# Kernel tuning notes

Measured on AMD Instinct MI355X. Metric: run time of the kernel, lower is better.

## Reference

```python
import jax, jax.numpy as jnp
import numpy as np

RANK = 24          # init: rank
WHITEN = True      # init: whiten
NS_ITERS = 5       # Newton-Schulz iterations for inverse matrix square root
EPS = 1e-5         # covariance jitter


def _ns_inv_sqrt(C, iters=NS_ITERS):
    # Newton-Schulz iteration computing C^{-1/2} for SPD C: (B, N, N).
    N = C.shape[-1]
    I = jnp.eye(N, dtype=C.dtype)
    normC = jnp.sqrt(jnp.sum(C * C, axis=(-2, -1), keepdims=True))  # Frobenius norm
    Y = C / normC
    Z = jnp.broadcast_to(I, C.shape)
    for _ in range(iters):
        T = 0.5 * (3.0 * I - Z @ Y)
        Y = Y @ T
        Z = T @ Z
    return Z / jnp.sqrt(normC)  # Z -> norm^{1/2} * C^{-1/2}


def _whiten(X):
    # X: (B, n, N) -> X @ Cov(X)^{-1/2}
    n = X.shape[-2]
    N = X.shape[-1]
    C = jnp.einsum('bnd,bne->bde', X, X) / n + EPS * jnp.eye(N, dtype=X.dtype)
    return X @ _ns_inv_sqrt(C)


def _procrustes_rotation(M):
    # M = S^T T (B, d, d); orthogonal R = U Vh minimizing ||S R - T||_F (Kabsch).
    U, _, Vh = jnp.linalg.svd(M, full_matrices=False)
    return U @ Vh


def _align(source, target, rank=RANK, whiten=WHITEN):
    S = _whiten(source) if whiten else source
    T = _whiten(target) if whiten else target
    N = S.shape[-1]
    if N <= 32:
        # full Procrustes
        R = _procrustes_rotation(jnp.einsum('bnd,bne->bde', S, T))
        aligned = S @ R
    else:
        # project to rank-r joint subspace, align there, lift back with
        # identity on the orthogonal complement: R = Q Rr Q^T + (I - Q Q^T)
        X = jnp.concatenate([S, T], axis=1)                 # (B, 2n, N)
        _, _, Vh = jnp.linalg.svd(X, full_matrices=False)    # Vh: (B, N', N)
        Q = jnp.swapaxes(Vh[:, :rank, :], -2, -1)            # (B, N, r)
        Sp = S @ Q                                           # (B, n, r)
        Tp = T @ Q
        Rr = _procrustes_rotation(jnp.einsum('bnr,bns->brs', Sp, Tp))  # (B, r, r) small SVD
        # aligned = S @ (Q Rr Q^T + I - Q Q^T) = S + Sp (Rr - I) Q^T
        aligned = S + Sp @ (Rr - jnp.eye(rank, dtype=S.dtype)) @ jnp.swapaxes(Q, -2, -1)
    return aligned


def setup_inputs() -> dict:
    key = jax.random.key(0)
    k1, k2 = jax.random.split(key)
    source = jax.random.normal(k1, (64, 512, 384), dtype=jnp.float32)
    target = jax.random.normal(k2, (64, 512, 384), dtype=jnp.float32)
    return {"source": source, "target": target}


def reference(source, target):
    aligned = _align(source, target)
    # diagnostic: mean cosine similarity between aligned and target rows
    cos = jnp.sum(aligned * target, axis=-1) / (
        jnp.linalg.norm(aligned, axis=-1) * jnp.linalg.norm(target, axis=-1) + 1e-8)
    cos_after = jnp.mean(cos)
    return aligned, cos_after
```

## Files before the change

### kernel.cpp

```cpp
#include <hip/hip_runtime.h>
#include <math.h>

static constexpr int BATCH = 64;
static constexpr int NR  = 512;
static constexpr int ND  = 384;
static constexpr int RK  = 24;
static constexpr int POLAR_ITERS = 36;
static constexpr int PNB = 32;
static constexpr long SZC = (long)BATCH * ND * ND;
static constexpr int SSTR = BATCH * RK;

#define MODE_PLAIN 0
#define MODE_COV   1
#define MODE_SCALE 3
#define MODE_ACC   4

typedef _Float16 half8 __attribute__((ext_vector_type(8)));
typedef _Float16 half4 __attribute__((ext_vector_type(4)));
typedef float floatx4 __attribute__((ext_vector_type(4)));

template<int TA>
__global__ __launch_bounds__(256)
void gemm_kernel(const float* __restrict__ Ag, const float* __restrict__ Bg,
                 float* __restrict__ Cg, int M, int N, int K,
                 long sA, long sB, long sC, int lda, int ldb, int ldc,
                 int mode, const float* __restrict__ scale, int sym, int tmask)
{
    const int batch = blockIdx.y;
    const int tilesN = N >> 7;
    int ti, tj;
    if (sym) {
        int idx = blockIdx.x;
        ti = 0; int rem = tilesN;
        while (idx >= rem) { idx -= rem; ti++; rem--; }
        tj = ti + idx;
    } else {
        tj = blockIdx.x % tilesN;
        ti = blockIdx.x / tilesN;
    }
    const int n0 = tj * 128, m0 = ti * 128;
    const float* A = Ag + (long)batch * sA;
    const float* Bm = Bg + (long)batch * sB;
    float* C = Cg + (long)batch * sC;

    __shared__ _Float16 Ah[128][40], Al[128][40];
    __shared__ _Float16 Bh[128][40], Bl[128][40];

    const int tid = threadIdx.x;
    const int wave = tid >> 6, lane = tid & 63;
    const int wm0 = (wave >> 1) * 64, wn0 = (wave & 1) * 64;
    const int fm = lane & 15;
    const int fq = lane >> 4;

    floatx4 acc[4][4];
#pragma unroll
    for (int i = 0; i < 4; i++)
#pragma unroll
        for (int j = 0; j < 4; j++) acc[i][j] = (floatx4){0.f, 0.f, 0.f, 0.f};

    for (int k0 = 0; k0 < K; k0 += 32) {
        if (TA == 0) {
#pragma unroll
            for (int q = 0; q < 4; q++) {
                int idx = tid + q * 256;
                int row = idx >> 3, kq = (idx & 7) * 4;
                float4 v = *(const float4*)&A[(long)(m0 + row) * lda + k0 + kq];
                if (tmask & 1) {
                    int gr = m0 + row, gc = k0 + kq;
                    v.x = ((gr == gc    ) ? 1.5f : 0.f) - 0.5f * v.x;
                    v.y = ((gr == gc + 1) ? 1.5f : 0.f) - 0.5f * v.y;
                    v.z = ((gr == gc + 2) ? 1.5f : 0.f) - 0.5f * v.z;
                    v.w = ((gr == gc + 3) ? 1.5f : 0.f) - 0.5f * v.w;
                }
                _Float16 h0 = (_Float16)v.x; _Float16 l0 = (_Float16)(v.x - (float)h0);
                _Float16 h1 = (_Float16)v.y; _Float16 l1 = (_Float16)(v.y - (float)h1);
                _Float16 h2 = (_Float16)v.z; _Float16 l2 = (_Float16)(v.z - (float)h2);
                _Float16 h3 = (_Float16)v.w; _Float16 l3 = (_Float16)(v.w - (float)h3);
                half4 hv, lv;
                hv[0] = h0; hv[1] = h1; hv[2] = h2; hv[3] = h3;
                lv[0] = l0; lv[1] = l1; lv[2] = l2; lv[3] = l3;
                *(half4*)&Ah[row][kq] = hv;
                *(half4*)&Al[row][kq] = lv;
            }
        } else {
            int m = tid & 127, kb = (tid >> 7) * 16;
            _Float16 hbuf[16], lbuf[16];
#pragma unroll
            for (int i = 0; i < 16; i++) {
                float v = A[(long)(k0 + kb + i) * lda + m0 + m];
                _Float16 hh = (_Float16)v;
                hbuf[i] = hh; lbuf[i] = (_Float16)(v - (float)hh);
            }
#pragma unroll
            for (int i = 0; i < 16; i += 4) {
                half4 hv, lv;
                hv[0] = hbuf[i]; hv[1] = hbuf[i + 1]; hv[2] = hbuf[i + 2]; hv[3] = hbuf[i + 3];
                lv[0] = lbuf[i]; lv[1] = lbuf[i + 1]; lv[2] = lbuf[i + 2]; lv[3] = lbuf[i + 3];
                *(half4*)&Ah[m][kb + i] = hv;
                *(half4*)&Al[m][kb + i] = lv;
            }
        }
        {
            int n = tid & 127, kb = (tid >> 7) * 16;
            _Float16 hbuf[16], lbuf[16];
#pragma unroll
            for (int i = 0; i < 16; i++) {
                float v = Bm[(long)(k0 + kb + i) * ldb + n0 + n];
                if (tmask & 2) v = (((k0 + kb + i) == (n0 + n)) ? 1.5f : 0.f) - 0.5f * v;
                _Float16 hh = (_Float16)v;
                hbuf[i] = hh; lbuf[i] = (_Float16)(v - (float)hh);
            }
#pragma unroll
            for (int i = 0; i < 16; i += 4) {
                half4 hv, lv;
                hv[0] = hbuf[i]; hv[1] = hbuf[i + 1]; hv[2] = hbuf[i + 2]; hv[3] = hbuf[i + 3];
                lv[0] = lbuf[i]; lv[1] = lbuf[i + 1]; lv[2] = lbuf[i + 2]; lv[3] = lbuf[i + 3];
                *(half4*)&Bh[n][kb + i] = hv;
                *(half4*)&Bl[n][kb + i] = lv;
            }
        }
        __syncthreads();

        half8 ah[4], alv[4], bh[4], blv[4];
#pragma unroll
        for (int mt = 0; mt < 4; mt++) {
            ah[mt]  = *(const half8*)&Ah[wm0 + mt * 16 + fm][fq * 8];
            alv[mt] = *(const half8*)&Al[wm0 + mt * 16 + fm][fq * 8];
        }
#pragma unroll
        for (int nt = 0; nt < 4; nt++) {
            bh[nt]  = *(const half8*)&Bh[wn0 + nt * 16 + fm][fq * 8];
            blv[nt] = *(const half8*)&Bl[wn0 + nt * 16 + fm][fq * 8];
        }
#pragma unroll
        for (int mt = 0; mt < 4; mt++) {
#pragma unroll
            for (int nt = 0; nt < 4; nt++) {
                floatx4 a = acc[mt][nt];
                a = __builtin_amdgcn_mfma_f32_16x16x32_f16(alv[mt], bh[nt], a, 0, 0, 0);
                a = __builtin_amdgcn_mfma_f32_16x16x32_f16(ah[mt], blv[nt], a, 0, 0, 0);
                a = __builtin_amdgcn_mfma_f32_16x16x32_f16(ah[mt], bh[nt], a, 0, 0, 0);
                acc[mt][nt] = a;
            }
        }
        __syncthreads();
    }

    float scl = 1.f;
    if (mode == MODE_SCALE) scl = 1.0f / sqrtf(scale[batch]);

#pragma unroll
    for (int mt = 0; mt < 4; mt++) {
#pragma unroll
        for (int nt = 0; nt < 4; nt++) {
            int gn = n0 + wn0 + nt * 16 + fm;
#pragma unroll
            for (int r = 0; r < 4; r++) {
                int gm = m0 + wm0 + mt * 16 + fq * 4 + r;
                float a = acc[mt][nt][r];
                float* cp = C + (long)gm * ldc + gn;
                float v = a;
                if (mode == MODE_COV)      v = a * (1.0f / 512.0f) + ((gm == gn) ? 1e-5f : 0.f);
                else if (mode == MODE_SCALE) v = a * scl;
                else if (mode == MODE_ACC) v = a + *cp;
                *cp = v;
                if (sym && ti != tj) {
                    float* cq = C + (long)gn * ldc + gm;
                    float vq = v;
                    if (mode == MODE_ACC) vq = a + *cq;
                    *cq = vq;
                }
            }
        }
    }
}

__global__ __launch_bounds__(256)
void frob_kernel(const float* __restrict__ Cm, float* __restrict__ nrm)
{
    int b = blockIdx.x;
    const float* p = Cm + (long)b * ND * ND;
    float s = 0.f;
    for (int i = threadIdx.x; i < ND * ND; i += 256) { float v = p[i]; s += v * v; }
    __shared__ float red[256];
    red[threadIdx.x] = s; __syncthreads();
    for (int off = 128; off > 0; off >>= 1) {
        if (threadIdx.x < off) red[threadIdx.x] += red[threadIdx.x + off];
        __syncthreads();
    }
    if (threadIdx.x == 0) nrm[b] = sqrtf(red[0]);
}

__global__ __launch_bounds__(256)
void initns_kernel(float* __restrict__ Mb, float* __restrict__ Z, const float* __restrict__ nrm)
{
    const int total = BATCH * ND * ND;
    for (int idx = blockIdx.x * 256 + threadIdx.x; idx < total; idx += gridDim.x * 256) {
        int b = idx / (ND * ND);
        int rem = idx - b * (ND * ND);
        int r = rem / ND, c = rem - r * ND;
        float v = Mb[idx] / nrm[b];
        Mb[idx] = v;
        Z[idx] = ((r == c) ? 1.5f : 0.f) - 0.5f * v;
    }
}

__device__ __forceinline__ float bred768(float v, float* red12, int t)
{
#pragma unroll
    for (int off = 32; off > 0; off >>= 1) v += __shfl_down(v, off);
    if ((t & 63) == 0) red12[t >> 6] = v;
    __syncthreads();
    float r = 0.f;
#pragma unroll
    for (int i = 0; i < 12; i++) r += red12[i];
    __syncthreads();
    return r;
}

__global__ __launch_bounds__(768)
void tridiag_panel(float* __restrict__ Gall, float* __restrict__ dA,
                   float* __restrict__ eA, float* __restrict__ tauA,
                   float* __restrict__ Wgall, int k0)
{
    int b = blockIdx.x;
    float* A = Gall + (long)b * ND * ND;
    float* Wg = Wgall + (long)b * (PNB * ND);
    float* d = dA + b * ND; float* e = eA + b * ND; float* tau = tauA + b * ND;
    const int t = threadIdx.x;
    const int h = (t >= ND) ? 1 : 0;
    const int c = t - h * ND;
    const int g = t % 96;
    const int s = t / 96;
    __shared__ float Ul[PNB][ND];
    __shared__ float Wl[PNB][ND];
    __shared__ float u_s[ND];
    __shared__ float pp4s[8][392];
    __shared__ float al[PNB], be[PNB];
    __shared__ float red12[12];
    __shared__ float s_tau;

    const int jcnt = min(PNB, ND - 2 - k0);

    for (int j = 0; j < jcnt; j++) {
        const int k = k0 + j;
        const int m = ND - 1 - k;
        float x = 0.f;
        if (!h && c < m) {
            const int kc = (k + 1) + c;
            x = A[(long)k * ND + kc];
#pragma unroll 4
            for (int l = 0; l < j; l++) {
                x -= Ul[l][k] * Wl[l][kc] + Wl[l][k] * Ul[l][kc];
            }
            u_s[c] = x;
        }
        float sigma = bred768(x * x, red12, t);
        if (t == 0) {
            float v0 = u_s[0];
            float normx = sqrtf(sigma);
            float alpha = (v0 >= 0.f) ? -normx : normx;
            float denom = sigma - alpha * v0;
            float tk = (denom > 1e-30f) ? 1.f / denom : 0.f;
            s_tau = tk;
            float diag = A[(long)k * ND + k];
            for (int l = 0; l < j; l++) diag -= 2.f * Ul[l][k] * Wl[l][k];
            e[k] = alpha; tau[k] = tk; d[k] = diag;
            u_s[0] = v0 - alpha;
        }
        __syncthreads();
        const float tk = s_tau;

        const int kk4 = (k + 1) & ~3;
        const int off = (k + 1) - kk4;
        const int ncol4 = 96 - (kk4 >> 2);
        if (g < ncol4) {
            const int ri0 = (m * s) >> 3;
            const int ri1 = (m * (s + 1)) >> 3;
            const float* base = A + (long)(k + 1) * ND + kk4 + 4 * g;
            floatx4 p4 = (floatx4){0.f, 0.f, 0.f, 0.f};
            int i = ri0;
            for (; i + 8 <= ri1; i += 8) {
                floatx4 a0 = *(const floatx4*)&base[(long)(i    ) * ND];
                floatx4 a1 = *(const floatx4*)&base[(long)(i + 1) * ND];
                floatx4 a2 = *(const floatx4*)&base[(long)(i + 2) * ND];
                floatx4 a3 = *(const floatx4*)&base[(long)(i + 3) * ND];
                floatx4 a4 = *(const floatx4*)&base[(long)(i + 4) * ND];
                floatx4 a5 = *(const floatx4*)&base[(long)(i + 5) * ND];
                floatx4 a6 = *(const floatx4*)&base[(long)(i + 6) * ND];
                floatx4 a7 = *(const floatx4*)&base[(long)(i + 7) * ND];
                p4 += a0 * u_s[i]     + a1 * u_s[i + 1] + a2 * u_s[i + 2] + a3 * u_s[i + 3]
                    + a4 * u_s[i + 4] + a5 * u_s[i + 5] + a6 * u_s[i + 6] + a7 * u_s[i + 7];
            }
            for (; i < ri1; i++) {
                floatx4 a0 = *(const floatx4*)&base[(long)i * ND];
                p4 += a0 * u_s[i];
            }
            *(floatx4*)&pp4s[s][4 * g] = p4;
        }
        {
            int wv = t >> 6, ln = t & 63;
            for (int l = wv; l < j; l += 12) {
                float sa = 0.f, sb = 0.f;
                const float* wrow = &Wl[l][k + 1];
                const float* urow = &Ul[l][k + 1];
                for (int i = ln; i < m; i += 64) { sa += wrow[i] * u_s[i]; sb += urow[i] * u_s[i]; }
#pragma unroll
                for (int off2 = 32; off2 > 0; off2 >>= 1) {
                    sa += __shfl_down(sa, off2); sb += __shfl_down(sb, off2);
                }
                if (ln == 0) { al[l] = sa; be[l] = sb; }
            }
        }
        __syncthreads();
        float contrib = 0.f, pc = 0.f;
        if (!h && c < m) {
            int ca = c + off;
            pc = pp4s[0][ca] + pp4s[1][ca] + pp4s[2][ca] + pp4s[3][ca]
               + pp4s[4][ca] + pp4s[5][ca] + pp4s[6][ca] + pp4s[7][ca];
            const int kc = (k + 1) + c;
#pragma unroll 4
            for (int l = 0; l < j; l++) {
                pc -= al[l] * Ul[l][kc] + be[l] * Wl[l][kc];
            }
            pc *= tk;
            contrib = u_s[c] * pc;
        }
        float dotup = bred768(contrib, red12, t);
        float sc = 0.5f * tk * dotup;
        if (!h && c < m) {
            const int kc = (k + 1) + c;
            float uv = u_s[c];
            float w = pc - sc * uv;
            Wl[j][kc] = w;
            Ul[j][kc] = uv;
            Wg[j * ND + kc] = w;
            A[(long)k * ND + kc] = uv;
        }
        __syncthreads();
    }
    if (k0 + PNB >= ND - 2 && t == 0) {
        float d0 = A[(long)(ND - 2) * ND + (ND - 2)];
        float e0 = A[(long)(ND - 2) * ND + (ND - 1)];
        float d1 = A[(long)(ND - 1) * ND + (ND - 1)];
        for (int l = 0; l < jcnt; l++) {
            float u0 = A[(long)(k0 + l) * ND + (ND - 2)];
            float u1 = A[(long)(k0 + l) * ND + (ND - 1)];
            float w0 = Wg[l * ND + (ND - 2)];
            float w1 = Wg[l * ND + (ND - 1)];
            d0 -= 2.f * u0 * w0;
            e0 -= u0 * w1 + w0 * u1;
            d1 -= 2.f * u1 * w1;
        }
        d[ND - 2] = d0; d[ND - 1] = d1; e[ND - 2] = e0;
        e[ND - 1] = 0.f; tau[ND - 2] = 0.f; tau[ND - 1] = 0.f;
    }
}

__global__ __launch_bounds__(256)
void syr2k_update(float* __restrict__ Gall, const float* __restrict__ Wgall, int k0)
{
    const int k1 = k0 + PNB;
    const int tiles = (ND - k1) >> 5;
    int b = blockIdx.y;
    int ti = blockIdx.x / tiles, tj = blockIdx.x % tiles;
    int i0 = k1 + ti * 32, c0 = k1 + tj * 32;
    float* A = Gall + (long)b * ND * ND;
    const float* Wg = Wgall + (long)b * (PNB * ND);

    __shared__ float Us[PNB][36], Ws[PNB][36], Uc[PNB][36], Wc[PNB][36];
    int t = threadIdx.x;
    for (int q = t; q < PNB * 8; q += 256) {
        int l = q >> 3, c4 = (q & 7) * 4;
        *(float4*)&Us[l][c4] = *(const float4*)&A[(long)(k0 + l) * ND + i0 + c4];
        *(float4*)&Ws[l][c4] = *(const float4*)&Wg[l * ND + i0 + c4];
        *(float4*)&Uc[l][c4] = *(const float4*)&A[(long)(k0 + l) * ND + c0 + c4];
        *(float4*)&Wc[l][c4] = *(const float4*)&Wg[l * ND + c0 + c4];
    }
    __syncthreads();
    int tr = t >> 4, tc = t & 15;
    float acc00 = 0.f, acc01 = 0.f, acc10 = 0.f, acc11 = 0.f;
#pragma unroll 4
    for (int l = 0; l < PNB; l++) {
        float ua0 = Us[l][tr * 2], ua1 = Us[l][tr * 2 + 1];
        float wa0 = Ws[l][tr * 2], wa1 = Ws[l][tr * 2 + 1];
        float ub0 = Uc[l][tc * 2], ub1 = Uc[l][tc * 2 + 1];
        float wb0 = Wc[l][tc * 2], wb1 = Wc[l][tc * 2 + 1];
        acc00 += ua0 * wb0 + wa0 * ub0;
        acc01 += ua0 * wb1 + wa0 * ub1;
        acc10 += ua1 * wb0 + wa1 * ub0;
        acc11 += ua1 * wb1 + wa1 * ub1;
    }
    {
        float* r0 = &A[(long)(i0 + tr * 2) * ND + c0 + tc * 2];
        float* r1 = r0 + ND;
        float2 o0 = *(const float2*)r0, o1 = *(const float2*)r1;
        o0.x -= acc00; o0.y -= acc01;
        o1.x -= acc10; o1.y -= acc11;
        *(float2*)r0 = o0; *(float2*)r1 = o1;
    }
}

__global__ __launch_bounds__(64)
void eigvals_kernel(const float* __restrict__ dA, const float* __restrict__ eA,
                    float* __restrict__ lamA)
{
    int b = blockIdx.x, t = threadIdx.x;
    __shared__ float2 de[ND];
    __shared__ float d_s[ND], ea[ND], red[64];
    for (int i = t; i < ND; i += 64) {
        float dv = dA[b * ND + i];
        float ev = eA[b * ND + i];
        float ep = (i > 0) ? eA[b * ND + i - 1] : 0.f;
        d_s[i] = dv; ea[i] = fabsf(ev);
        de[i] = make_float2(dv, ep * ep + 1e-38f);
    }
    __syncthreads();
    float lo = 1e30f, hi = -1e30f;
    for (int i = t; i < ND; i += 64) {
        float r = ea[i] + ((i > 0) ? ea[i - 1] : 0.f);
        lo = fminf(lo, d_s[i] - r); hi = fmaxf(hi, d_s[i] + r);
    }
    red[t] = lo; __syncthreads();
    for (int off = 32; off > 0; off >>= 1) {
        if (t < off) red[t] = fminf(red[t], red[t + off]);
        __syncthreads();
    }
    lo = red[0]; __syncthreads();
    red[t] = hi; __syncthreads();
    for (int off = 32; off > 0; off >>= 1) {
        if (t < off) red[t] = fmaxf(red[t], red[t + off]);
        __syncthreads();
    }
    hi = red[0];
    if (t < RK) {
        int idx = ND - 1 - t;
        float a = lo, c = hi;
        for (int it = 0; it < 42; it++) {
            float mid = 0.5f * (a + c);
            int cnt = 0;
            float qinv = 0.f;
            for (int i = 0; i < ND; i += 8) {
                float2 v0 = de[i    ], v1 = de[i + 1], v2 = de[i + 2], v3 = de[i + 3];
                float2 v4 = de[i + 4], v5 = de[i + 5], v6 = de[i + 6], v7 = de[i + 7];
                float q;
                q = (v0.x - mid) - v0.y * qinv; cnt += (q < 0.f); qinv = __builtin_amdgcn_rcpf(q);
                q = (v1.x - mid) - v1.y * qinv; cnt += (q < 0.f); qinv = __builtin_amdgcn_rcpf(q);
                q = (v2.x - mid) - v2.y * qinv; cnt += (q < 0.f); qinv = __builtin_amdgcn_rcpf(q);
                q = (v3.x - mid) - v3.y * qinv; cnt += (q < 0.f); qinv = __builtin_amdgcn_rcpf(q);
                q = (v4.x - mid) - v4.y * qinv; cnt += (q < 0.f); qinv = __builtin_amdgcn_rcpf(q);
                q = (v5.x - mid) - v5.y * qinv; cnt += (q < 0.f); qinv = __builtin_amdgcn_rcpf(q);
                q = (v6.x - mid) - v6.y * qinv; cnt += (q < 0.f); qinv = __builtin_amdgcn_rcpf(q);
                q = (v7.x - mid) - v7.y * qinv; cnt += (q < 0.f); qinv = __builtin_amdgcn_rcpf(q);
            }
            if (cnt > idx) c = mid; else a = mid;
        }
        lamA[b * RK + t] = 0.5f * (a + c);
    }
}

__global__ __launch_bounds__(64)
void invit_kernel(const float* __restrict__ dA, const float* __restrict__ eA,
                  const float* __restrict__ lamA, float* __restrict__ scr)
{
    int b = blockIdx.x, t = threadIdx.x;
    __shared__ float d[ND], e[ND];
    __shared__ float ua[ND][RK], ub[ND][RK], uc[ND][RK];
    __shared__ float y[ND][RK];
    for (int i = t; i < ND; i += 64) { d[i] = dA[b * ND + i]; e[i] = eA[b * ND + i]; }
    __syncthreads();
    if (t >= RK) return;
    const int s = b * RK + t;
// ... 182 lines not shown
    int b = blockIdx.x, t = threadIdx.x;
    __shared__ float Sb[128][RK + 1], Tb[128][RK + 1];
    __shared__ float Xm[RK][RK + 1], Bm[RK][RK + 1], Mm[RK][RK + 1];
    __shared__ float red[256];

    float accM[3] = {0.f, 0.f, 0.f};
    for (int c = 0; c < 4; c++) {
        for (int l = t; l < 128 * RK; l += 256) {
            int row = l / RK, colj = l - row * RK;
            Sb[row][colj] = Sp[(long)b * NR * RK + (long)(c * 128 + row) * RK + colj];
            Tb[row][colj] = Tp[(long)b * NR * RK + (long)(c * 128 + row) * RK + colj];
        }
        __syncthreads();
        for (int q = 0; q < 3; q++) {
            int e = t + q * 256;
            if (e < RK * RK) {
                int r = e / RK, s2 = e - r * RK;
                float a = 0.f;
                for (int n = 0; n < 128; n++) a += Sb[n][r] * Tb[n][s2];
                accM[q] += a;
            }
        }
        __syncthreads();
    }
    float ss = 0.f;
    for (int q = 0; q < 3; q++) {
        int e = t + q * 256;
        if (e < RK * RK) {
            int r = e / RK, s2 = e - r * RK;
            Mm[r][s2] = accM[q];
            ss += accM[q] * accM[q];
        }
    }
    red[t] = ss; __syncthreads();
    for (int off = 128; off > 0; off >>= 1) {
        if (t < off) red[t] += red[t + off];
        __syncthreads();
    }
    float fro = sqrtf(red[0]);
    float inv = (fro > 1e-30f) ? 1.f / fro : 0.f;
    for (int q = 0; q < 3; q++) {
        int e = t + q * 256;
        if (e < RK * RK) { int r = e / RK, s2 = e - r * RK; Xm[r][s2] = Mm[r][s2] * inv; }
    }
    __syncthreads();
    for (int it = 0; it < POLAR_ITERS; it++) {
        for (int q = 0; q < 3; q++) {
            int e = t + q * 256;
            if (e < RK * RK) {
                int r = e / RK, s2 = e - r * RK;
                float a = 0.f;
                for (int k = 0; k < RK; k++) a += Xm[k][r] * Xm[k][s2];
                Bm[r][s2] = a;
            }
        }
        __syncthreads();
        for (int q = 0; q < 3; q++) {
            int e = t + q * 256;
            if (e < RK * RK) {
                int r = e / RK, s2 = e - r * RK;
                float a = 0.f;
                for (int k = 0; k < RK; k++) a += Xm[r][k] * Bm[k][s2];
                Mm[r][s2] = 1.5f * Xm[r][s2] - 0.5f * a;
            }
        }
        __syncthreads();
        for (int q = 0; q < 3; q++) {
            int e = t + q * 256;
            if (e < RK * RK) { int r = e / RK, s2 = e - r * RK; Xm[r][s2] = Mm[r][s2]; }
        }
        __syncthreads();
    }
    for (int q = 0; q < 3; q++) {
        int e = t + q * 256;
        if (e < RK * RK) {
            int r = e / RK, s2 = e - r * RK;
            RmI[(long)b * RK * RK + e] = Xm[r][s2] - ((r == s2) ? 1.f : 0.f);
        }
    }
}

__global__ __launch_bounds__(256)
void align_kernel(const float* __restrict__ Sw, const float* __restrict__ Sp,
                  const float* __restrict__ RmI, const float* __restrict__ Qall,
                  float* __restrict__ out)
{
    int b = blockIdx.y;
    int r0 = blockIdx.x * 64;
    int t = threadIdx.x;
    __shared__ float Qs[ND][RK + 1];
    __shared__ float Rm[RK][RK + 1];
    __shared__ float Ss[64][RK + 1];
    __shared__ float W[64][RK + 1];

    for (int l = t; l < ND * RK; l += 256) {
        int i = l / RK, j = l - i * RK;
        Qs[i][j] = Qall[(long)b * ND * RK + l];
    }
    for (int l = t; l < RK * RK; l += 256) {
        int i = l / RK, j = l - i * RK;
        Rm[i][j] = RmI[(long)b * RK * RK + l];
    }
    for (int l = t; l < 64 * RK; l += 256) {
        int i = l / RK, j = l - i * RK;
        Ss[i][j] = Sp[(long)b * NR * RK + (long)(r0 + i) * RK + j];
    }
    __syncthreads();
    for (int l = t; l < 64 * RK; l += 256) {
        int r = l / RK, j = l - r * RK;
        float a = 0.f;
        for (int k = 0; k < RK; k++) a += Ss[r][k] * Rm[k][j];
        W[r][j] = a;
    }
    __syncthreads();
    for (int r = 0; r < 64; r++) {
        for (int c = t; c < ND; c += 256) {
            float a = Sw[(long)b * NR * ND + (long)(r0 + r) * ND + c];
            float s2 = 0.f;
#pragma unroll
            for (int j = 0; j < RK; j++) s2 += W[r][j] * Qs[c][j];
            out[(long)b * NR * ND + (long)(r0 + r) * ND + c] = a + s2;
        }
    }
}

__global__ __launch_bounds__(256)
void cos_kernel(const float* __restrict__ out, const float* __restrict__ tgt,
                float* __restrict__ acc)
{
    int row = blockIdx.x * 4 + (threadIdx.x >> 6);
    int lane = threadIdx.x & 63;
    const float* a = out + (long)row * ND;
    const float* tg = tgt + (long)row * ND;
    float sd = 0.f, sa = 0.f, st = 0.f;
    for (int i = lane; i < ND; i += 64) {
        float av = a[i], tv = tg[i];
        sd += av * tv; sa += av * av; st += tv * tv;
    }
#pragma unroll
    for (int off = 32; off > 0; off >>= 1) {
        sd += __shfl_down(sd, off); sa += __shfl_down(sa, off); st += __shfl_down(st, off);
    }
    __shared__ float part[4];
    if (lane == 0) part[threadIdx.x >> 6] = sd / (sqrtf(sa) * sqrtf(st) + 1e-8f);
    __syncthreads();
    if (threadIdx.x == 0) atomicAdd(acc, part[0] + part[1] + part[2] + part[3]);
}

__global__ void finalize_kernel(const float* __restrict__ acc, float* __restrict__ out)
{
    out[0] = acc[0] / 32768.0f;
}

static inline void launch_gemm(int TA, const float* A, const float* Bm, float* C,
                               int M, int N, int K, long sA, long sB, long sC,
                               int lda, int ldb, int ldc, int mode,
                               const float* scale, int sym, int tmask, hipStream_t stream)
{
    int tiles;
    if (sym) { int tn = N >> 7; tiles = tn * (tn + 1) / 2; }
    else tiles = (M / 128) * (N / 128);
    dim3 grid(tiles, BATCH);
    if (TA)
        gemm_kernel<1><<<grid, dim3(256), 0, stream>>>(A, Bm, C, M, N, K, sA, sB, sC, lda, ldb, ldc, mode, scale, sym, tmask);
    else
        gemm_kernel<0><<<grid, dim3(256), 0, stream>>>(A, Bm, C, M, N, K, sA, sB, sC, lda, ldb, ldc, mode, scale, sym, tmask);
}

extern "C" void kernel_launch(void* const* d_in, const int* in_sizes, int n_in,
                              void* d_out, int out_size, void* d_ws, size_t ws_size,
                              hipStream_t stream)
{
    const float* src = (const float*)d_in[0];
    const float* tgt = (const float*)d_in[1];
    float* out = (float*)d_out;
    float* ws = (float*)d_ws;

    float* A0 = ws;
    float* A1 = ws + 1 * SZC;
    float* A2 = ws + 2 * SZC;
    float* A3 = ws + 3 * SZC;
    float* A4 = ws + 4 * SZC;
    float* S5 = ws + 5 * SZC;
    float* nrm_s = S5;
    float* nrm_t = S5 + 64;
    float* dd = S5 + 128;
    float* ee = dd + BATCH * ND;
    float* tt = ee + BATCH * ND;
    float* lam = tt + BATCH * ND;
    float* accp = lam + BATCH * RK;

    float* Tm = out;
    float* SW = A0;
    float* TW = A0 + (long)BATCH * NR * ND;
    float* B4 = TW;
    float* G  = A3;
    float* scr = A4;
    float* Qp  = A4 + 6L * ND * SSTR;
    float* Spp = Qp + (long)BATCH * ND * RK;
    float* Tpp = Spp + (long)BATCH * NR * RK;
    float* Rp  = Tpp + (long)BATCH * NR * RK;
    float* Wg  = Rp + (long)BATCH * RK * RK;
    float* yarr = scr + 5L * ND * SSTR;

    const long sXin = (long)NR * ND;
    const long sSq  = (long)ND * ND;

    launch_gemm(1, src, src, A3, ND, ND, NR, sXin, sXin, sSq, ND, ND, ND, MODE_COV, nullptr, 1, 0, stream);
    frob_kernel<<<BATCH, 256, 0, stream>>>(A3, nrm_s);
    initns_kernel<<<dim3(2048), 256, 0, stream>>>(A3, A4, nrm_s);
    launch_gemm(0, A3, A3, Tm, ND, ND, ND, sSq, sSq, sSq, ND, ND, ND, MODE_PLAIN, nullptr, 1, 3, stream);
    launch_gemm(0, A3, Tm, A0, ND, ND, ND, sSq, sSq, sSq, ND, ND, ND, MODE_PLAIN, nullptr, 1, 0, stream);
    launch_gemm(0, A0, A4, A3, ND, ND, ND, sSq, sSq, sSq, ND, ND, ND, MODE_PLAIN, nullptr, 1, 1, stream);
    launch_gemm(0, A0, A0, Tm, ND, ND, ND, sSq, sSq, sSq, ND, ND, ND, MODE_PLAIN, nullptr, 1, 3, stream);
    launch_gemm(0, A0, Tm, A4, ND, ND, ND, sSq, sSq, sSq, ND, ND, ND, MODE_PLAIN, nullptr, 1, 0, stream);
    launch_gemm(0, A4, A3, A0, ND, ND, ND, sSq, sSq, sSq, ND, ND, ND, MODE_PLAIN, nullptr, 1, 1, stream);
    launch_gemm(0, A4, A4, Tm, ND, ND, ND, sSq, sSq, sSq, ND, ND, ND, MODE_PLAIN, nullptr, 1, 3, stream);
    launch_gemm(0, A4, Tm, A3, ND, ND, ND, sSq, sSq, sSq, ND, ND, ND, MODE_PLAIN, nullptr, 1, 0, stream);
    launch_gemm(0, A3, A0, A4, ND, ND, ND, sSq, sSq, sSq, ND, ND, ND, MODE_PLAIN, nullptr, 1, 1, stream);
    launch_gemm(0, A3, A3, Tm, ND, ND, ND, sSq, sSq, sSq, ND, ND, ND, MODE_PLAIN, nullptr, 1, 3, stream);
    launch_gemm(0, A3, Tm, A0, ND, ND, ND, sSq, sSq, sSq, ND, ND, ND, MODE_PLAIN, nullptr, 1, 0, stream);
    launch_gemm(0, A0, A4, A3, ND, ND, ND, sSq, sSq, sSq, ND, ND, ND, MODE_PLAIN, nullptr, 1, 1, stream);
    launch_gemm(0, src, A3, SW, NR, ND, ND, sXin, sSq, sXin, ND, ND, ND, MODE_SCALE, nrm_s, 0, 0, stream);

    launch_gemm(1, tgt, tgt, A3, ND, ND, NR, sXin, sXin, sSq, ND, ND, ND, MODE_COV, nullptr, 1, 0, stream);
    frob_kernel<<<BATCH, 256, 0, stream>>>(A3, nrm_t);
    initns_kernel<<<dim3(2048), 256, 0, stream>>>(A3, A4, nrm_t);
    launch_gemm(0, A3, A3, Tm, ND, ND, ND, sSq, sSq, sSq, ND, ND, ND, MODE_PLAIN, nullptr, 1, 3, stream);
    launch_gemm(0, A3, Tm, B4, ND, ND, ND, sSq, sSq, sSq, ND, ND, ND, MODE_PLAIN, nullptr, 1, 0, stream);
    launch_gemm(0, B4, A4, A3, ND, ND, ND, sSq, sSq, sSq, ND, ND, ND, MODE_PLAIN, nullptr, 1, 1, stream);
    launch_gemm(0, B4, B4, Tm, ND, ND, ND, sSq, sSq, sSq, ND, ND, ND, MODE_PLAIN, nullptr, 1, 3, stream);
    launch_gemm(0, B4, Tm, A4, ND, ND, ND, sSq, sSq, sSq, ND, ND, ND, MODE_PLAIN, nullptr, 1, 0, stream);
    launch_gemm(0, A4, A3, B4, ND, ND, ND, sSq, sSq, sSq, ND, ND, ND, MODE_PLAIN, nullptr, 1, 1, stream);
    launch_gemm(0, A4, A4, Tm, ND, ND, ND, sSq, sSq, sSq, ND, ND, ND, MODE_PLAIN, nullptr, 1, 3, stream);
    launch_gemm(0, A4, Tm, A3, ND, ND, ND, sSq, sSq, sSq, ND, ND, ND, MODE_PLAIN, nullptr, 1, 0, stream);
    launch_gemm(0, A3, B4, A4, ND, ND, ND, sSq, sSq, sSq, ND, ND, ND, MODE_PLAIN, nullptr, 1, 1, stream);
    launch_gemm(0, A3, A3, Tm, ND, ND, ND, sSq, sSq, sSq, ND, ND, ND, MODE_PLAIN, nullptr, 1, 3, stream);
    launch_gemm(0, A3, Tm, B4, ND, ND, ND, sSq, sSq, sSq, ND, ND, ND, MODE_PLAIN, nullptr, 1, 0, stream);
    launch_gemm(0, B4, A4, A3, ND, ND, ND, sSq, sSq, sSq, ND, ND, ND, MODE_PLAIN, nullptr, 1, 1, stream);
    launch_gemm(0, tgt, A3, TW, NR, ND, ND, sXin, sSq, sXin, ND, ND, ND, MODE_SCALE, nrm_t, 0, 0, stream);

    launch_gemm(1, SW, SW, G, ND, ND, NR, sXin, sXin, sSq, ND, ND, ND, MODE_PLAIN, nullptr, 1, 0, stream);
    launch_gemm(1, TW, TW, G, ND, ND, NR, sXin, sXin, sSq, ND, ND, ND, MODE_ACC, nullptr, 1, 0, stream);
    for (int p = 0; p < ND / PNB; p++) {
        tridiag_panel<<<BATCH, 768, 0, stream>>>(G, dd, ee, tt, Wg, p * PNB);
        int k1 = (p + 1) * PNB;
        if (k1 < ND - 2) {
            int tiles = (ND - k1) >> 5;
            syr2k_update<<<dim3(tiles * tiles, BATCH), 256, 0, stream>>>(G, Wg, p * PNB);
        }
    }
    eigvals_kernel<<<BATCH, 64, 0, stream>>>(dd, ee, lam);
    invit_kernel<<<BATCH, 64, 0, stream>>>(dd, ee, lam, scr);
    orthbt_kernel<<<BATCH, 384, 0, stream>>>(yarr, G, tt, Qp);
    proj_kernel<<<dim3(2, BATCH), 256, 0, stream>>>(SW, Qp, Spp);
    proj_kernel<<<dim3(2, BATCH), 256, 0, stream>>>(TW, Qp, Tpp);
    polar_kernel<<<BATCH, 256, 0, stream>>>(Spp, Tpp, Rp);
    align_kernel<<<dim3(8, BATCH), 256, 0, stream>>>(SW, Spp, Rp, Qp, out);
    hipMemsetAsync((void*)accp, 0, 4, stream);
    cos_kernel<<<dim3(8192), 256, 0, stream>>>(out, tgt, accp);
    finalize_kernel<<<1, 1, 0, stream>>>(accp, out + (long)BATCH * NR * ND);
    (void)in_sizes; (void)n_in; (void)out_size; (void)ws_size;
}
```

Measured before the change: 5.640 ms.

## Compute panel symmetric matvec from upper triangle with mirrored row dots

```diff
diff --git a/kernel.cpp b/kernel.cpp
--- a/kernel.cpp
+++ b/kernel.cpp
@@ -218,6 +218,39 @@
     return r;
 }
 
+__device__ __forceinline__ float sym_rowdot(const float* __restrict__ A,
+                                            const float* __restrict__ u_s,
+                                            int k, int r, int h2)
+{
+    const int rAbs = k + 1 + r;
+    const float* row = A + (long)rAbs * ND;
+    const int S = rAbs + 1;
+    int base = (S & ~3) + 4 * h2;
+    float accr = 0.f;
+    if (base < S) {
+        floatx4 a0 = *(const floatx4*)&row[base];
+#pragma unroll
+        for (int jj = 0; jj < 4; jj++) {
+            int C = base + jj;
+            if (C >= S) accr += a0[jj] * u_s[C - (k + 1)];
+        }
+        base += 8;
+    }
+    for (; base <= 372; base += 16) {
+        floatx4 a0 = *(const floatx4*)&row[base];
+        floatx4 a1 = *(const floatx4*)&row[base + 8];
+        int ui = base - (k + 1);
+        accr += a0[0] * u_s[ui]     + a0[1] * u_s[ui + 1] + a0[2] * u_s[ui + 2] + a0[3] * u_s[ui + 3]
+              + a1[0] * u_s[ui + 8] + a1[1] * u_s[ui + 9] + a1[2] * u_s[ui + 10] + a1[3] * u_s[ui + 11];
+    }
+    for (; base <= 380; base += 8) {
+        floatx4 a0 = *(const floatx4*)&row[base];
+        int ui = base - (k + 1);
+        accr += a0[0] * u_s[ui] + a0[1] * u_s[ui + 1] + a0[2] * u_s[ui + 2] + a0[3] * u_s[ui + 3];
+    }
+    return accr;
+}
+
 __global__ __launch_bounds__(768)
 void tridiag_panel(float* __restrict__ Gall, float* __restrict__ dA,
                    float* __restrict__ eA, float* __restrict__ tauA,
@@ -236,6 +269,7 @@
     __shared__ float Wl[PNB][ND];
     __shared__ float u_s[ND];
     __shared__ float pp4s[8][392];
+    __shared__ float mirp[ND][2];
     __shared__ float al[PNB], be[PNB];
     __shared__ float red12[12];
     __shared__ float s_tau;
@@ -278,9 +312,12 @@
             const int ri0 = (m * s) >> 3;
             const int ri1 = (m * (s + 1)) >> 3;
             const float* base = A + (long)(k + 1) * ND + kk4 + 4 * g;
+            const int C0 = kk4 + 4 * g;
+            const int I0 = C0 - (k + 1);
             floatx4 p4 = (floatx4){0.f, 0.f, 0.f, 0.f};
+            int iEnd = I0 + 1; if (iEnd > ri1) iEnd = ri1;
             int i = ri0;
-            for (; i + 8 <= ri1; i += 8) {
+            for (; i + 8 <= iEnd; i += 8) {
                 floatx4 a0 = *(const floatx4*)&base[(long)(i    ) * ND];
                 floatx4 a1 = *(const floatx4*)&base[(long)(i + 1) * ND];
                 floatx4 a2 = *(const floatx4*)&base[(long)(i + 2) * ND];
@@ -292,11 +329,33 @@
                 p4 += a0 * u_s[i]     + a1 * u_s[i + 1] + a2 * u_s[i + 2] + a3 * u_s[i + 3]
                     + a4 * u_s[i + 4] + a5 * u_s[i + 5] + a6 * u_s[i + 6] + a7 * u_s[i + 7];
             }
-            for (; i < ri1; i++) {
+            for (; i < iEnd; i++) {
                 floatx4 a0 = *(const floatx4*)&base[(long)i * ND];
                 p4 += a0 * u_s[i];
             }
+            int iBnd = I0 + 4; if (iBnd > ri1) iBnd = ri1;
+            for (; i < iBnd; i++) {
+                floatx4 a0 = *(const floatx4*)&base[(long)i * ND];
+                const int R = k + 1 + i;
+                a0[0] = (C0     >= R) ? a0[0] : 0.f;
+                a0[1] = (C0 + 1 >= R) ? a0[1] : 0.f;
+                a0[2] = (C0 + 2 >= R) ? a0[2] : 0.f;
+                a0[3] = (C0 + 3 >= R) ? a0[3] : 0.f;
+                p4 += a0 * u_s[i];
+            }
             *(floatx4*)&pp4s[s][4 * g] = p4;
+        }
+        {
+            const int p2 = t >> 1, h2 = t & 1;
+            const int rB = m - 1 - p2;
+            if (rB >= p2) {
+                float mrA = sym_rowdot(A, u_s, k, p2, h2);
+                mirp[p2][h2] = mrA;
+                if (rB > p2) {
+                    float mrB = sym_rowdot(A, u_s, k, rB, h2);
+                    mirp[rB][h2] = mrB;
+                }
+            }
         }
         {
             int wv = t >> 6, ln = t & 63;
@@ -317,7 +376,8 @@
         if (!h && c < m) {
             int ca = c + off;
             pc = pp4s[0][ca] + pp4s[1][ca] + pp4s[2][ca] + pp4s[3][ca]
-               + pp4s[4][ca] + pp4s[5][ca] + pp4s[6][ca] + pp4s[7][ca];
+               + pp4s[4][ca] + pp4s[5][ca] + pp4s[6][ca] + pp4s[7][ca]
+               + mirp[c][0] + mirp[c][1];
             const int kc = (k + 1) + c;
 #pragma unroll 4
             for (int l = 0; l < j; l++) {
```

Result: slower. 6.627 ms (+17.5%).

## Batch source/target GEMMs into dual launches and register-prefetch next K tile

Applied to the files above, without the earlier changes.

```diff
diff --git a/kernel.cpp b/kernel.cpp
--- a/kernel.cpp
+++ b/kernel.cpp
@@ -22,11 +22,26 @@
 template<int TA>
 __global__ __launch_bounds__(256)
 void gemm_kernel(const float* __restrict__ Ag, const float* __restrict__ Bg,
-                 float* __restrict__ Cg, int M, int N, int K,
+                 float* __restrict__ Cg,
+                 const float* __restrict__ Ag2, const float* __restrict__ Bg2,
+                 float* __restrict__ Cg2,
+                 int M, int N, int K,
                  long sA, long sB, long sC, int lda, int ldb, int ldc,
-                 int mode, const float* __restrict__ scale, int sym, int tmask)
-{
-    const int batch = blockIdx.y;
+                 int mode, const float* __restrict__ scale,
+                 int mode2, const float* __restrict__ scale2,
+                 int sym, int tmask, int tmask2)
+{
+    const int by = blockIdx.y;
+    int bloc;
+    const float* A; const float* Bm; float* C;
+    if (by < BATCH) {
+        bloc = by;
+        A = Ag + (long)bloc * sA; Bm = Bg + (long)bloc * sB; C = Cg + (long)bloc * sC;
+    } else {
+        bloc = by - BATCH;
+        A = Ag2 + (long)bloc * sA; Bm = Bg2 + (long)bloc * sB; C = Cg2 + (long)bloc * sC;
+        mode = mode2; scale = scale2; tmask = tmask2;
+    }
     const int tilesN = N >> 7;
     int ti, tj;
     if (sym) {
@@ -39,9 +54,6 @@
         ti = blockIdx.x / tilesN;
     }
     const int n0 = tj * 128, m0 = ti * 128;
-    const float* A = Ag + (long)batch * sA;
-    const float* Bm = Bg + (long)batch * sB;
-    float* C = Cg + (long)batch * sC;
 
     __shared__ _Float16 Ah[128][40], Al[128][40];
     __shared__ _Float16 Bh[128][40], Bl[128][40];
@@ -58,13 +70,37 @@
 #pragma unroll
         for (int j = 0; j < 4; j++) acc[i][j] = (floatx4){0.f, 0.f, 0.f, 0.f};
 
+    float4 pA4[4];
+    float  pAs[16];
+    float  pBs[16];
+
+    if (TA == 0) {
+#pragma unroll
+        for (int q = 0; q < 4; q++) {
+            int idx = tid + q * 256;
+            int row = idx >> 3, kq = (idx & 7) * 4;
+            pA4[q] = *(const float4*)&A[(long)(m0 + row) * lda + kq];
+        }
+    } else {
+        int m = tid & 127, kb = (tid >> 7) * 16;
+#pragma unroll
+        for (int i = 0; i < 16; i++)
+            pAs[i] = A[(long)(kb + i) * lda + m0 + m];
+    }
+    {
+        int n = tid & 127, kb = (tid >> 7) * 16;
+#pragma unroll
+        for (int i = 0; i < 16; i++)
+            pBs[i] = Bm[(long)(kb + i) * ldb + n0 + n];
+    }
+
     for (int k0 = 0; k0 < K; k0 += 32) {
         if (TA == 0) {
 #pragma unroll
             for (int q = 0; q < 4; q++) {
                 int idx = tid + q * 256;
                 int row = idx >> 3, kq = (idx & 7) * 4;
-                float4 v = *(const float4*)&A[(long)(m0 + row) * lda + k0 + kq];
+                float4 v = pA4[q];
                 if (tmask & 1) {
                     int gr = m0 + row, gc = k0 + kq;
                     v.x = ((gr == gc    ) ? 1.5f : 0.f) - 0.5f * v.x;
@@ -84,37 +120,31 @@
             }
         } else {
             int m = tid & 127, kb = (tid >> 7) * 16;
-            _Float16 hbuf[16], lbuf[16];
-#pragma unroll
-            for (int i = 0; i < 16; i++) {
-                float v = A[(long)(k0 + kb + i) * lda + m0 + m];
-                _Float16 hh = (_Float16)v;
-                hbuf[i] = hh; lbuf[i] = (_Float16)(v - (float)hh);
-            }
 #pragma unroll
             for (int i = 0; i < 16; i += 4) {
                 half4 hv, lv;
-                hv[0] = hbuf[i]; hv[1] = hbuf[i + 1]; hv[2] = hbuf[i + 2]; hv[3] = hbuf[i + 3];
-                lv[0] = lbuf[i]; lv[1] = lbuf[i + 1]; lv[2] = lbuf[i + 2]; lv[3] = lbuf[i + 3];
+#pragma unroll
+                for (int jj = 0; jj < 4; jj++) {
+                    float v = pAs[i + jj];
+                    _Float16 hh = (_Float16)v;
+                    hv[jj] = hh; lv[jj] = (_Float16)(v - (float)hh);
+                }
                 *(half4*)&Ah[m][kb + i] = hv;
                 *(half4*)&Al[m][kb + i] = lv;
             }
         }
         {
             int n = tid & 127, kb = (tid >> 7) * 16;
-            _Float16 hbuf[16], lbuf[16];
-#pragma unroll
-            for (int i = 0; i < 16; i++) {
-                float v = Bm[(long)(k0 + kb + i) * ldb + n0 + n];
-                if (tmask & 2) v = (((k0 + kb + i) == (n0 + n)) ? 1.5f : 0.f) - 0.5f * v;
-                _Float16 hh = (_Float16)v;
-                hbuf[i] = hh; lbuf[i] = (_Float16)(v - (float)hh);
-            }
 #pragma unroll
             for (int i = 0; i < 16; i += 4) {
                 half4 hv, lv;
-                hv[0] = hbuf[i]; hv[1] = hbuf[i + 1]; hv[2] = hbuf[i + 2]; hv[3] = hbuf[i + 3];
-                lv[0] = lbuf[i]; lv[1] = lbuf[i + 1]; lv[2] = lbuf[i + 2]; lv[3] = lbuf[i + 3];
+#pragma unroll
+                for (int jj = 0; jj < 4; jj++) {
+                    float v = pBs[i + jj];
+                    if (tmask & 2) v = (((k0 + kb + i + jj) == (n0 + n)) ? 1.5f : 0.f) - 0.5f * v;
+                    _Float16 hh = (_Float16)v;
+                    hv[jj] = hh; lv[jj] = (_Float16)(v - (float)hh);
+                }
                 *(half4*)&Bh[n][kb + i] = hv;
                 *(half4*)&Bl[n][kb + i] = lv;
             }
@@ -132,6 +162,30 @@
             bh[nt]  = *(const half8*)&Bh[wn0 + nt * 16 + fm][fq * 8];
             blv[nt] = *(const half8*)&Bl[wn0 + nt * 16 + fm][fq * 8];
         }
+
+        if (k0 + 32 < K) {
+            const int kn = k0 + 32;
+            if (TA == 0) {
+#pragma unroll
+                for (int q = 0; q < 4; q++) {
+                    int idx = tid + q * 256;
+                    int row = idx >> 3, kq = (idx & 7) * 4;
+                    pA4[q] = *(const float4*)&A[(long)(m0 + row) * lda + kn + kq];
+                }
+            } else {
+                int m = tid & 127, kb = (tid >> 7) * 16;
+#pragma unroll
+                for (int i = 0; i < 16; i++)
+                    pAs[i] = A[(long)(kn + kb + i) * lda + m0 + m];
+            }
+            {
+                int n = tid & 127, kb = (tid >> 7) * 16;
+#pragma unroll
+                for (int i = 0; i < 16; i++)
+                    pBs[i] = Bm[(long)(kn + kb + i) * ldb + n0 + n];
+            }
+        }
+
 #pragma unroll
         for (int mt = 0; mt < 4; mt++) {
 #pragma unroll
@@ -147,7 +201,7 @@
     }
 
     float scl = 1.f;
-    if (mode == MODE_SCALE) scl = 1.0f / sqrtf(scale[batch]);
+    if (mode == MODE_SCALE) scl = 1.0f / sqrtf(scale[bloc]);
 
 #pragma unroll
     for (int mt = 0; mt < 4; mt++) {
@@ -176,10 +230,12 @@
 }
 
 __global__ __launch_bounds__(256)
-void frob_kernel(const float* __restrict__ Cm, float* __restrict__ nrm)
+void frob_kernel(const float* __restrict__ Cm1, const float* __restrict__ Cm2,
+                 float* __restrict__ nrm)
 {
     int b = blockIdx.x;
-    const float* p = Cm + (long)b * ND * ND;
+    const float* p = (b < BATCH) ? (Cm1 + (long)b * ND * ND)
+                                 : (Cm2 + (long)(b - BATCH) * ND * ND);
     float s = 0.f;
     for (int i = threadIdx.x; i < ND * ND; i += 256) { float v = p[i]; s += v * v; }
     __shared__ float red[256];
@@ -806,19 +862,31 @@
     out[0] = acc[0] / 32768.0f;
 }
 
-static inline void launch_gemm(int TA, const float* A, const float* Bm, float* C,
-                               int M, int N, int K, long sA, long sB, long sC,
-                               int lda, int ldb, int ldc, int mode,
-                               const float* scale, int sym, int tmask, hipStream_t stream)
+static inline void launch_gd(int TA,
+    const float* A1p, const float* B1p, float* C1p, int mode1, const float* sc1, int tm1,
+    const float* A2p, const float* B2p, float* C2p, int mode2, const float* sc2, int tm2,
+    int nbat, int M, int N, int K, long sA, long sB, long sC,
+    int lda, int ldb, int ldc, int sym, hipStream_t stream)
 {
     int tiles;
     if (sym) { int tn = N >> 7; tiles = tn * (tn + 1) / 2; }
     else tiles = (M / 128) * (N / 128);
-    dim3 grid(tiles, BATCH);
+    dim3 grid(tiles, nbat);
     if (TA)
-        gemm_kernel<1><<<grid, dim3(256), 0, stream>>>(A, Bm, C, M, N, K, sA, sB, sC, lda, ldb, ldc, mode, scale, sym, tmask);
+        gemm_kernel<1><<<grid, dim3(256), 0, stream>>>(A1p, B1p, C1p, A2p, B2p, C2p,
+            M, N, K, sA, sB, sC, lda, ldb, ldc, mode1, sc1, mode2, sc2, sym, tm1, tm2);
     else
-        gemm_kernel<0><<<grid, dim3(256), 0, stream>>>(A, Bm, C, M, N, K, sA, sB, sC, lda, ldb, ldc, mode, scale, sym, tmask);
+        gemm_kernel<0><<<grid, dim3(256), 0, stream>>>(A1p, B1p, C1p, A2p, B2p, C2p,
+            M, N, K, sA, sB, sC, lda, ldb, ldc, mode1, sc1, mode2, sc2, sym, tm1, tm2);
+}
+
+static inline void launch_g1(int TA, const float* Ap, const float* Bp, float* Cp,
+    int mode, const float* sc, int tm,
+    int M, int N, int K, long sA, long sB, long sC,
+    int lda, int ldb, int ldc, int sym, hipStream_t stream)
+{
+    launch_gd(TA, Ap, Bp, Cp, mode, sc, tm, Ap, Bp, Cp, mode, sc, tm,
+              BATCH, M, N, K, sA, sB, sC, lda, ldb, ldc, sym, stream);
 }
 
 extern "C" void kernel_launch(void* const* d_in, const int* in_sizes, int n_in,
@@ -831,8 +899,6 @@
     float* ws = (float*)d_ws;
 
     float* A0 = ws;
-    float* A1 = ws + 1 * SZC;
-    float* A2 = ws + 2 * SZC;
     float* A3 = ws + 3 * SZC;
     float* A4 = ws + 4 * SZC;
     float* S5 = ws + 5 * SZC;
@@ -847,7 +913,7 @@
     float* Tm = out;
     float* SW = A0;
     float* TW = A0 + (long)BATCH * NR * ND;
-    float* B4 = TW;
+    float* C1 = TW;
     float* G  = A3;
     float* scr = A4;
     float* Qp  = A4 + 6L * ND * SSTR;
@@ -860,48 +926,65 @@
     const long sXin = (long)NR * ND;
     const long sSq  = (long)ND * ND;
 
-    launch_gemm(1, src, src, A3, ND, ND, NR, sXin, sXin, sSq, ND, ND, ND, MODE_COV, nullptr, 1, 0, stream);
-    frob_kernel<<<BATCH, 256, 0, stream>>>(A3, nrm_s);
+    launch_gd(1, src, src, A3, MODE_COV, nullptr, 0,
+                 tgt, tgt, C1, MODE_COV, nullptr, 0,
+              128, ND, ND, NR, sXin, sXin, sSq, ND, ND, ND, 1, stream);
+    frob_kernel<<<dim3(128), 256, 0, stream>>>(A3, C1, nrm_s);
+
     initns_kernel<<<dim3(2048), 256, 0, stream>>>(A3, A4, nrm_s);
-    launch_gemm(0, A3, A3, Tm, ND, ND, ND, sSq, sSq, sSq, ND, ND, ND, MODE_PLAIN, nullptr, 1, 3, stream);
-    launch_gemm(0, A3, Tm, A0, ND, ND, ND, sSq, sSq, sSq, ND, ND, ND, MODE_PLAIN, nullptr, 1, 0, stream);
-    launch_gemm(0, A0, A4, A3, ND, ND, ND, sSq, sSq, sSq, ND, ND, ND, MODE_PLAIN, nullptr, 1, 1, stream);
-    launch_gemm(0, A0, A0, Tm, ND, ND, ND, sSq, sSq, sSq, ND, ND, ND, MODE_PLAIN, nullptr, 1, 3, stream);
-    launch_gemm(0, A0, Tm, A4, ND, ND, ND, sSq, sSq, sSq, ND, ND, ND, MODE_PLAIN, nullptr, 1, 0, stream);
-    launch_gemm(0, A4, A3, A0, ND, ND, ND, sSq, sSq, sSq, ND, ND, ND, MODE_PLAIN, nullptr, 1, 1, stream);
-    launch_gemm(0, A4, A4, Tm, ND, ND, ND, sSq, sSq, sSq, ND, ND, ND, MODE_PLAIN, nullptr, 1, 3, stream);
-    launch_gemm(0, A4, Tm, A3, ND, ND, ND, sSq, sSq, sSq, ND, ND, ND, MODE_PLAIN, nullptr, 1, 0, stream);
-    launch_gemm(0, A3, A0, A4, ND, ND, ND, sSq, sSq, sSq, ND, ND, ND, MODE_PLAIN, nullptr, 1, 1, stream);
-    launch_gemm(0, A3, A3, Tm, ND, ND, ND, sSq, sSq, sSq, ND, ND, ND, MODE_PLAIN, nullptr, 1, 3, stream);
-    launch_gemm(0, A3, Tm, A0, ND, ND, ND, sSq, sSq, sSq, ND, ND, ND, MODE_PLAIN, nullptr, 1, 0, stream);
-    launch_gemm(0, A0, A4, A3, ND, ND, ND, sSq, sSq, sSq, ND, ND, ND, MODE_PLAIN, nullptr, 1, 1, stream);
-    launch_gemm(0, src, A3, SW, NR, ND, ND, sXin, sSq, sXin, ND, ND, ND, MODE_SCALE, nrm_s, 0, 0, stream);
-
-    launch_gemm(1, tgt, tgt, A3, ND, ND, NR, sXin, sXin, sSq, ND, ND, ND, MODE_COV, nullptr, 1, 0, stream);
-    frob_kernel<<<BATCH, 256, 0, stream>>>(A3, nrm_t);
-    initns_kernel<<<dim3(2048), 256, 0, stream>>>(A3, A4, nrm_t);
-    launch_gemm(0, A3, A3, Tm, ND, ND, ND, sSq, sSq, sSq, ND, ND, ND, MODE_PLAIN, nullptr, 1, 3, stream);
-    launch_gemm(0, A3, Tm, B4, ND, ND, ND, sSq, sSq, sSq, ND, ND, ND, MODE_PLAIN, nullptr, 1, 0, stream);
-    launch_gemm(0, B4, A4, A3, ND, ND, ND, sSq, sSq, sSq, ND, ND, ND, MODE_PLAIN, nullptr, 1, 1, stream);
-    launch_gemm(0, B4, B4, Tm, ND, ND, ND, sSq, sSq, sSq, ND, ND, ND, MODE_PLAIN, nullptr, 1, 3, stream);
-    launch_gemm(0, B4, Tm, A4, ND, ND, ND, sSq, sSq, sSq, ND, ND, ND, MODE_PLAIN, nullptr, 1, 0, stream);
-    launch_gemm(0, A4, A3, B4, ND, ND, ND, sSq, sSq, sSq, ND, ND, ND, MODE_PLAIN, nullptr, 1, 1, stream);
-    launch_gemm(0, A4, A4, Tm, ND, ND, ND, sSq, sSq, sSq, ND, ND, ND, MODE_PLAIN, nullptr, 1, 3, stream);
-    launch_gemm(0, A4, Tm, A3, ND, ND, ND, sSq, sSq, sSq, ND, ND, ND, MODE_PLAIN, nullptr, 1, 0, stream);
-    launch_gemm(0, A3, B4, A4, ND, ND, ND, sSq, sSq, sSq, ND, ND, ND, MODE_PLAIN, nullptr, 1, 1, stream);
-    launch_gemm(0, A3, A3, Tm, ND, ND, ND, sSq, sSq, sSq, ND, ND, ND, MODE_PLAIN, nullptr, 1, 3, stream);
-    launch_gemm(0, A3, Tm, B4, ND, ND, ND, sSq, sSq, sSq, ND, ND, ND, MODE_PLAIN, nullptr, 1, 0, stream);
-    launch_gemm(0, B4, A4, A3, ND, ND, ND, sSq, sSq, sSq, ND, ND, ND, MODE_PLAIN, nullptr, 1, 1, stream);
-    launch_gemm(0, tgt, A3, TW, NR, ND, ND, sXin, sSq, sXin, ND, ND, ND, MODE_SCALE, nrm_t, 0, 0, stream);
-
-    launch_gemm(1, SW, SW, G, ND, ND, NR, sXin, sXin, sSq, ND, ND, ND, MODE_PLAIN, nullptr, 1, 0, stream);
-    launch_gemm(1, TW, TW, G, ND, ND, NR, sXin, sXin, sSq, ND, ND, ND, MODE_ACC, nullptr, 1, 0, stream);
+    launch_g1(0, A3, A3, Tm, MODE_PLAIN, nullptr, 3, ND, ND, ND, sSq, sSq, sSq, ND, ND, ND, 1, stream);
+    launch_g1(0, A3, Tm, A0, MODE_PLAIN, nullptr, 0, ND, ND, ND, sSq, sSq, sSq, ND, ND, ND, 1, stream);
+    launch_gd(0, A0, A4, A3, MODE_PLAIN, nullptr, 1,
+                 A0, A0, Tm, MODE_PLAIN, nullptr, 3,
+              128, ND, ND, ND, sSq, sSq, sSq, ND, ND, ND, 1, stream);
+    launch_g1(0, A0, Tm, A4, MODE_PLAIN, nullptr, 0, ND, ND, ND, sSq, sSq, sSq, ND, ND, ND, 1, stream);
+    launch_gd(0, A4, A3, A0, MODE_PLAIN, nullptr, 1,
+                 A4, A4, Tm, MODE_PLAIN, nullptr, 3,
+              128, ND, ND, ND, sSq, sSq, sSq, ND, ND, ND, 1, stream);
+    launch_g1(0, A4, Tm, A3, MODE_PLAIN, nullptr, 0, ND, ND, ND, sSq, sSq, sSq, ND, ND, ND, 1, stream);
+    launch_gd(0, A3, A0, A4, MODE_PLAIN, nullptr, 1,
+                 A3, A3, Tm, MODE_PLAIN, nullptr, 3,
+              128, ND, ND, ND, sSq, sSq, sSq, ND, ND, ND, 1, stream);
+    launch_g1(0, A3, Tm, A0, MODE_PLAIN, nullptr, 0, ND, ND, ND, sSq, sSq, sSq, ND, ND, ND, 1, stream);
+    launch_g1(0, A0, A4, A3, MODE_PLAIN, nullptr, 1, ND, ND, ND, sSq, sSq, sSq, ND, ND, ND, 1, stream);
+
+    initns_kernel<<<dim3(2048), 256, 0, stream>>>(C1, A0, nrm_t);
+    launch_g1(0, C1, C1, Tm, MODE_PLAIN, nullptr, 3, ND, ND, ND, sSq, sSq, sSq, ND, ND, ND, 1, stream);
+    launch_g1(0, C1, Tm, A4, MODE_PLAIN, nullptr, 0, ND, ND, ND, sSq, sSq, sSq, ND, ND, ND, 1, stream);
+    launch_gd(0, A4, A0, C1, MODE_PLAIN, nullptr, 1,
+                 A4, A4, Tm, MODE_PLAIN, nullptr, 3,
+              128, ND, ND, ND, sSq, sSq, sSq, ND, ND, ND, 1, stream);
+    launch_g1(0, A4, Tm, A0, MODE_PLAIN, nullptr, 0, ND, ND, ND, sSq, sSq, sSq, ND, ND, ND, 1, stream);
+    launch_gd(0, A0, C1, A4, MODE_PLAIN, nullptr, 1,
+                 A0, A0, Tm, MODE_PLAIN, nullptr, 3,
+              128, ND, ND, ND, sSq, sSq, sSq, ND, ND, ND, 1, stream);
+    launch_g1(0, A0, Tm, C1, MODE_PLAIN, nullptr, 0, ND, ND, ND, sSq, sSq, sSq, ND, ND, ND, 1, stream);
+    launch_gd(0, C1, A4, A0, MODE_PLAIN, nullptr, 1,
+                 C1, C1, Tm, MODE_PLAIN, nullptr, 3,
+              128, ND, ND, ND, sSq, sSq, sSq, ND, ND, ND, 1, stream);
+    launch_g1(0, C1, Tm, A4, MODE_PLAIN, nullptr, 0, ND, ND, ND, sSq, sSq, sSq, ND, ND, ND, 1, stream);
+    launch_g1(0, A4, A0, Tm, MODE_PLAIN, nullptr, 1, ND, ND, ND, sSq, sSq, sSq, ND, ND, ND, 1, stream);
+
+    launch_gd(0, src, A3, SW, MODE_SCALE, nrm_s, 0,
+                 tgt, Tm, TW, MODE_SCALE, nrm_t, 0,
+              128, NR, ND, ND, sXin, sSq, sXin, ND, ND, ND, 0, stream);
+
+    launch_g1(1, SW, SW, G, MODE_PLAIN, nullptr, 0, ND, ND, NR, sXin, sXin, sSq, ND, ND, ND, 1, stream);
+    launch_g1(1, TW, TW, G, MODE_ACC,   nullptr, 0, ND, ND, NR, sXin, sXin, sSq, ND, ND, ND, 1, stream);
+
     for (int p = 0; p < ND / PNB; p++) {
-        tridiag_panel<<<BATCH, 768, 0, stream>>>(G, dd, ee, tt, Wg, p * PNB);
+        int k0 = p * PNB;
+        if (p < 2) {
+            tridiag_panel<<<dim3(32), 768, 0, stream>>>(G, dd, ee, tt, Wg, k0);
+            tridiag_panel<<<dim3(32), 768, 0, stream>>>(G + 32L * sSq, dd + 32 * ND,
+                ee + 32 * ND, tt + 32 * ND, Wg + 32L * PNB * ND, k0);
+        } else {
+            tridiag_panel<<<dim3(BATCH), 768, 0, stream>>>(G, dd, ee, tt, Wg, k0);
+        }
         int k1 = (p + 1) * PNB;
         if (k1 < ND - 2) {
             int tiles = (ND - k1) >> 5;
-            syr2k_update<<<dim3(tiles * tiles, BATCH), 256, 0, stream>>>(G, Wg, p * PNB);
+            syr2k_update<<<dim3(tiles * tiles, BATCH), 256, 0, stream>>>(G, Wg, k0);
         }
     }
     eigvals_kernel<<<BATCH, 64, 0, stream>>>(dd, ee, lam);
```

Result: no change. 5.587 ms (-1.0%).
